# Kernel tuning notes

Hardware: AMD Instinct MI355X
Metric: run time of the kernel (lower is better)

## Reference

```python
import jax, jax.numpy as jnp
import numpy as np

K = 512
D = 256


def setup_inputs() -> dict:
    key = jax.random.key(0)
    k1, k2 = jax.random.split(key)
    x = jax.random.normal(k1, (64, D, 32, 32), dtype=jnp.float32)
    # nn.Embedding(K, D) init: uniform(-1/K, 1/K)
    emb = jax.random.uniform(k2, (K, D), dtype=jnp.float32, minval=-1.0 / K, maxval=1.0 / K)
    return {"x": x, "emb": emb}


def reference(x, emb):
    # encoder is identity: z_e_x = x, shape [B, D, H, W]
    B, Dd, H, W = x.shape
    z_e = jnp.transpose(x, (0, 2, 3, 1))           # [B, H, W, D]
    z_flat = z_e.reshape(-1, Dd)                    # [N, D]
    # squared euclidean distances to codebook: ||z||^2 + ||e||^2 - 2 z.e
    dist = (jnp.sum(z_flat * z_flat, axis=1, keepdims=True)
            + jnp.sum(emb * emb, axis=1)[None, :]
            - 2.0 * z_flat @ emb.T)                 # [N, K]
    idx = jnp.argmin(dist, axis=1)                  # [N]
    codes = emb[idx]                                # [N, D] gather
    codes = codes.reshape(B, H, W, Dd)
    # straight-through quantized output (value == codes)
    z_q_st = z_e + jax.lax.stop_gradient(codes - z_e)
    z_q_st = jnp.transpose(z_q_st, (0, 3, 1, 2))    # [B, D, H, W]
    # z_q_x_bar: gathered from live codebook (grads flow to emb)
    z_q_bar = jnp.transpose(codes, (0, 3, 1, 2))    # [B, D, H, W]
    # decoder is identity: x_tilde = z_q_st
    return (z_q_st, x, z_q_bar)
```

## Files before the change

kernel.cpp:

```cpp
#include <hip/hip_runtime.h>


#define B_  64
#define D_  256
#define HW_ 1024
#define K_  512

typedef __attribute__((ext_vector_type(8))) short short8;
typedef __attribute__((ext_vector_type(4))) float f32x4;

__device__ unsigned short g_ebf[K_ * D_];
__device__ float g_e2[K_];
__device__ float g_embT[D_ * K_];
__device__ int   g_idx[B_ * HW_];

__device__ __forceinline__ unsigned short f2bf(float f) {
    unsigned u = __float_as_uint(f);
    u += 0x7fffu + ((u >> 16) & 1u);
    return (unsigned short)(u >> 16);
}

__global__ void prep(const float* __restrict__ emb) {
    const int t   = threadIdx.x;
    const int row = blockIdx.x * 8 + (t >> 5);
    const int c0  = (t & 31) * 8;
    const float* rp = emb + row * D_ + c0;
    float4 a = *(const float4*)rp;
    float4 b = *(const float4*)(rp + 4);
    short8 v;
    v[0] = (short)f2bf(a.x); v[1] = (short)f2bf(a.y);
    v[2] = (short)f2bf(a.z); v[3] = (short)f2bf(a.w);
    v[4] = (short)f2bf(b.x); v[5] = (short)f2bf(b.y);
    v[6] = (short)f2bf(b.z); v[7] = (short)f2bf(b.w);
    *(short8*)(g_ebf + row * D_ + c0) = v;
    g_embT[(c0 + 0) * K_ + row] = a.x;
    g_embT[(c0 + 1) * K_ + row] = a.y;
    g_embT[(c0 + 2) * K_ + row] = a.z;
    g_embT[(c0 + 3) * K_ + row] = a.w;
    g_embT[(c0 + 4) * K_ + row] = b.x;
    g_embT[(c0 + 5) * K_ + row] = b.y;
    g_embT[(c0 + 6) * K_ + row] = b.z;
    g_embT[(c0 + 7) * K_ + row] = b.w;
    float ps = a.x*a.x + a.y*a.y + a.z*a.z + a.w*a.w
             + b.x*b.x + b.y*b.y + b.z*b.z + b.w*b.w;
    ps += __shfl_xor(ps, 1);  ps += __shfl_xor(ps, 2);
    ps += __shfl_xor(ps, 4);  ps += __shfl_xor(ps, 8);
    ps += __shfl_xor(ps, 16);
    if ((t & 31) == 0) g_e2[row] = ps;
}

__global__ __launch_bounds__(128, 4)
void vq_argmin(const float* __restrict__ x) {
    __shared__ float zc[4][32][32];
    __shared__ float mval[2][32];
    __shared__ int   midx[2][32];

    const int t   = threadIdx.x;
    const int w   = t >> 6;
    const int l   = t & 63;
    const int blk = blockIdx.x;
    const int b   = blk >> 5;
    const int hw0 = (blk & 31) << 5;
    const float* xb = x + ((size_t)b * D_) * HW_ + hw0;

    short8 zb[2][8];
    for (int r = 0; r < 2; ++r) {
#pragma unroll
        for (int gg = 0; gg < 2; ++gg) {
            const int g = 4 * r + 2 * w + gg;
#pragma unroll
            for (int it = 0; it < 4; ++it) {
                const float* gp = xb + (size_t)(32 * g + 8 * it + (l >> 3)) * HW_ + (l & 7) * 4;
                float* lp = &zc[g & 3][8 * it][0];
                __builtin_amdgcn_global_load_lds(
                    (const __attribute__((address_space(1))) unsigned int*)gp,
                    (__attribute__((address_space(3))) unsigned int*)lp,
                    16, 0, 0);
            }
        }
        __syncthreads();
#pragma unroll
        for (int g4 = 0; g4 < 4; ++g4) {
            const int g = 4 * r + g4;
#pragma unroll
            for (int t2 = 0; t2 < 2; ++t2) {
                const int p = 16 * t2 + (l & 15);
                short8 f;
#pragma unroll
                for (int j = 0; j < 8; ++j)
                    f[j] = (short)f2bf(zc[g4][(l >> 4) * 8 + j][p]);
                zb[t2][g] = f;
            }
        }
        __syncthreads();
    }

    float minv0 = 3.0e38f, minv1 = 3.0e38f;
    int   mini0 = 0,       mini1 = 0;
    short8 ea[8], eb[8];
    f32x4  e2a, e2b;
    const int ctbase = w * 16;

#define LOADE(buf, e2r, ct) do {                                              \
        const unsigned short* _p = g_ebf + ((ct) * 16 + (l & 15)) * D_        \
                                   + (l >> 4) * 8;                            \
        _Pragma("unroll")                                                     \
        for (int s = 0; s < 8; ++s) buf[s] = *(const short8*)(_p + s * 32);   \
        e2r = *(const f32x4*)(g_e2 + (ct) * 16 + (l >> 4) * 4);               \
    } while (0)

#define PROC(buf, e2v, ct) do {                                               \
        f32x4 a0 = {0.f, 0.f, 0.f, 0.f}, a1 = {0.f, 0.f, 0.f, 0.f};          \
        _Pragma("unroll")                                                     \
        for (int s = 0; s < 8; ++s) {                                         \
            a0 = __builtin_amdgcn_mfma_f32_16x16x32_bf16(buf[s], zb[0][s], a0, 0, 0, 0); \
            a1 = __builtin_amdgcn_mfma_f32_16x16x32_bf16(buf[s], zb[1][s], a1, 0, 0, 0); \
        }                                                                     \
        _Pragma("unroll")                                                     \
        for (int r = 0; r < 4; ++r) {                                         \
            const int code = (ct) * 16 + (l >> 4) * 4 + r;                    \
            const float s0 = e2v[r] - 2.0f * a0[r];                           \
            const float s1 = e2v[r] - 2.0f * a1[r];                           \
            if (s0 < minv0) { minv0 = s0; mini0 = code; }                     \
            if (s1 < minv1) { minv1 = s1; mini1 = code; }                     \
        }                                                                     \
    } while (0)

    LOADE(ea, e2a, ctbase);
    for (int c = 0; c < 16; c += 2) {
        LOADE(eb, e2b, ctbase + c + 1);
        PROC(ea, e2a, ctbase + c);
        const int cn = (c + 2 < 16) ? (ctbase + c + 2) : ctbase;
        LOADE(ea, e2a, cn);
        PROC(eb, e2b, ctbase + c + 1);
    }

    {
        float ov; int oi;
        ov = __shfl_xor(minv0, 16); oi = __shfl_xor(mini0, 16);
        if (ov < minv0 || (ov == minv0 && oi < mini0)) { minv0 = ov; mini0 = oi; }
        ov = __shfl_xor(minv0, 32); oi = __shfl_xor(mini0, 32);
        if (ov < minv0 || (ov == minv0 && oi < mini0)) { minv0 = ov; mini0 = oi; }
        ov = __shfl_xor(minv1, 16); oi = __shfl_xor(mini1, 16);
        if (ov < minv1 || (ov == minv1 && oi < mini1)) { minv1 = ov; mini1 = oi; }
        ov = __shfl_xor(minv1, 32); oi = __shfl_xor(mini1, 32);
        if (ov < minv1 || (ov == minv1 && oi < mini1)) { minv1 = ov; mini1 = oi; }
    }
    if ((l >> 4) == 0) {
        mval[w][l & 15]        = minv0; midx[w][l & 15]        = mini0;
        mval[w][16 + (l & 15)] = minv1; midx[w][16 + (l & 15)] = mini1;
    }
    __syncthreads();
    if (t < 32) {
        const float v0 = mval[0][t], v1 = mval[1][t];
        g_idx[b * HW_ + hw0 + t] = (v1 < v0) ? midx[1][t] : midx[0][t];
    }
}

__global__ __launch_bounds__(256)
void vq_scatter(const float* __restrict__ x, float* __restrict__ out0,
                float* __restrict__ out1, float* __restrict__ out2) {
    const int t   = threadIdx.x;
    const int blk = blockIdx.x;
    const int b   = blk >> 4;
    const int d0  = (blk & 15) << 4;
    const int4 mi = *(const int4*)(g_idx + b * HW_ + 4 * t);
    const size_t base = ((size_t)b * D_ + d0) * HW_ + 4 * t;
    const float* xp = x + base;
    float* p0 = out0 + base;
    float* p1 = out1 + base;
    float* p2 = out2 + base;
#pragma unroll 4
    for (int r = 0; r < 16; ++r) {
        const float* et = g_embT + (size_t)(d0 + r) * K_;
        const size_t off = (size_t)r * HW_;
        f32x4 xv = *(const f32x4*)(xp + off);
        f32x4 cv;
        cv[0] = et[mi.x]; cv[1] = et[mi.y];
        cv[2] = et[mi.z]; cv[3] = et[mi.w];
        __builtin_nontemporal_store(xv, (f32x4*)(p1 + off));
        __builtin_nontemporal_store(cv, (f32x4*)(p0 + off));
        __builtin_nontemporal_store(cv, (f32x4*)(p2 + off));
    }
}

extern "C" void kernel_launch(void* const* d_in, const int* in_sizes, int n_in,
                              void* d_out, int out_size, void* d_ws, size_t ws_size,
                              hipStream_t stream) {
    const float* x   = (const float*)d_in[0];
    const float* emb = (const float*)d_in[1];
    float* out0 = (float*)d_out;
    float* out1 = out0 + (size_t)16777216;
    float* out2 = out0 + (size_t)33554432;

    prep<<<64, 256, 0, stream>>>(emb);
    vq_argmin<<<2048, 128, 0, stream>>>(x);
    vq_scatter<<<1024, 256, 0, stream>>>(x, out0, out1, out2);
}
```

Before: 319.1 us.

## Stage codebook in swizzled LDS with double buffering; cache embT rows in scatter

The argmin kernel now uses 256-thread blocks covering 64 positions. Each wave owns 16 positions, and all four waves share a double-buffered, XOR-swizzled LDS copy of each 32-code bf16 codebook chunk, which is loaded asynchronously into LDS. Previously each wave fetched half the codebook straight from global memory into registers, and the result needed a cross-wave reduction through shared memory. The scatter kernel now copies an 8-row slice of the transposed codebook into LDS so its random gathers hit LDS instead of global memory, with twice as many blocks. The trade-offs are a block barrier per chunk and a higher LDS footprint per block.

```diff
diff --git a/kernel.cpp b/kernel.cpp
--- a/kernel.cpp
+++ b/kernel.cpp
@@ -49,135 +49,127 @@
     if ((t & 31) == 0) g_e2[row] = ps;
 }
 
-__global__ __launch_bounds__(128, 4)
+__global__ __launch_bounds__(256, 4)
 void vq_argmin(const float* __restrict__ x) {
-    __shared__ float zc[4][32][32];
-    __shared__ float mval[2][32];
-    __shared__ int   midx[2][32];
+    __shared__ unsigned short cb[2][32 * 256];
 
     const int t   = threadIdx.x;
     const int w   = t >> 6;
     const int l   = t & 63;
     const int blk = blockIdx.x;
-    const int b   = blk >> 5;
-    const int hw0 = (blk & 31) << 5;
+    const int b   = blk >> 4;
+    const int hw0 = (blk & 15) << 6;
     const float* xb = x + ((size_t)b * D_) * HW_ + hw0;
 
-    short8 zb[2][8];
-    for (int r = 0; r < 2; ++r) {
+    short8 zb[8];
+    float* xt = (float*)&cb[0][0];
+    for (int R = 0; R < 4; ++R) {
 #pragma unroll
-        for (int gg = 0; gg < 2; ++gg) {
-            const int g = 4 * r + 2 * w + gg;
-#pragma unroll
-            for (int it = 0; it < 4; ++it) {
-                const float* gp = xb + (size_t)(32 * g + 8 * it + (l >> 3)) * HW_ + (l & 7) * 4;
-                float* lp = &zc[g & 3][8 * it][0];
-                __builtin_amdgcn_global_load_lds(
-                    (const __attribute__((address_space(1))) unsigned int*)gp,
-                    (__attribute__((address_space(3))) unsigned int*)lp,
-                    16, 0, 0);
-            }
+        for (int k2 = 0; k2 < 4; ++k2) {
+            const int k  = 4 * w + k2;
+            const int dr = 4 * k + (l >> 4);
+            const float* gp = xb + (size_t)(64 * R + dr) * HW_ + (l & 15) * 4;
+            float* lp = xt + 256 * k;
+            __builtin_amdgcn_global_load_lds(
+                (const __attribute__((address_space(1))) unsigned int*)gp,
+                (__attribute__((address_space(3))) unsigned int*)lp, 16, 0, 0);
         }
         __syncthreads();
 #pragma unroll
-        for (int g4 = 0; g4 < 4; ++g4) {
-            const int g = 4 * r + g4;
+        for (int h = 0; h < 2; ++h) {
+            short8 f;
 #pragma unroll
-            for (int t2 = 0; t2 < 2; ++t2) {
-                const int p = 16 * t2 + (l & 15);
-                short8 f;
+            for (int j = 0; j < 8; ++j) {
+                const int dl = h * 32 + (l >> 4) * 8 + j;
+                f[j] = (short)f2bf(xt[dl * 64 + 16 * w + (l & 15)]);
+            }
+            zb[2 * R + h] = f;
+        }
+        __syncthreads();
+    }
+
+#define STAGEC(cc, bb) do {                                                   \
+        _Pragma("unroll")                                                     \
+        for (int k2 = 0; k2 < 4; ++k2) {                                      \
+            const int k  = 4 * w + k2;                                        \
+            const int rl = 2 * k + (l >> 5);        \
+            const unsigned short* gp = g_ebf + ((cc) * 32 + rl) * 256         \
+                                       + (((l & 31) ^ (rl & 7)) << 3);        \
+            unsigned short* lp = &cb[bb][512 * k];                            \
+            __builtin_amdgcn_global_load_lds(                                 \
+                (const __attribute__((address_space(1))) unsigned int*)gp,    \
+                (__attribute__((address_space(3))) unsigned int*)lp, 16, 0, 0);\
+        }                                                                     \
+    } while (0)
+
+    float minv = 3.0e38f;
+    int   mini = 0;
+
+    STAGEC(0, 0);
+    __syncthreads();
+    for (int c = 0; c < 16; ++c) {
+        if (c + 1 < 16) STAGEC(c + 1, (c + 1) & 1);
+        const unsigned short* cbuf = cb[c & 1];
 #pragma unroll
-                for (int j = 0; j < 8; ++j)
-                    f[j] = (short)f2bf(zc[g4][(l >> 4) * 8 + j][p]);
-                zb[t2][g] = f;
+        for (int ct2 = 0; ct2 < 2; ++ct2) {
+            f32x4 acc = {0.f, 0.f, 0.f, 0.f};
+            const int cr = ct2 * 16 + (l & 15);
+#pragma unroll
+            for (int s = 0; s < 8; ++s) {
+                const int unit = ((l >> 4) + 4 * s) ^ (cr & 7);
+                short8 a = *(const short8*)(cbuf + cr * 256 + unit * 8);
+                acc = __builtin_amdgcn_mfma_f32_16x16x32_bf16(a, zb[s], acc, 0, 0, 0);
+            }
+            const int cbase = 32 * c + 16 * ct2 + (l >> 4) * 4;
+            f32x4 e2v = *(const f32x4*)(g_e2 + cbase);
+#pragma unroll
+            for (int r = 0; r < 4; ++r) {
+                const float sv = e2v[r] - 2.0f * acc[r];
+                if (sv < minv) { minv = sv; mini = cbase + r; }
             }
         }
         __syncthreads();
     }
 
-    float minv0 = 3.0e38f, minv1 = 3.0e38f;
-    int   mini0 = 0,       mini1 = 0;
-    short8 ea[8], eb[8];
-    f32x4  e2a, e2b;
-    const int ctbase = w * 16;
-
-#define LOADE(buf, e2r, ct) do {                                              \
-        const unsigned short* _p = g_ebf + ((ct) * 16 + (l & 15)) * D_        \
-                                   + (l >> 4) * 8;                            \
-        _Pragma("unroll")                                                     \
-        for (int s = 0; s < 8; ++s) buf[s] = *(const short8*)(_p + s * 32);   \
-        e2r = *(const f32x4*)(g_e2 + (ct) * 16 + (l >> 4) * 4);               \
-    } while (0)
-
-#define PROC(buf, e2v, ct) do {                                               \
-        f32x4 a0 = {0.f, 0.f, 0.f, 0.f}, a1 = {0.f, 0.f, 0.f, 0.f};          \
-        _Pragma("unroll")                                                     \
-        for (int s = 0; s < 8; ++s) {                                         \
-            a0 = __builtin_amdgcn_mfma_f32_16x16x32_bf16(buf[s], zb[0][s], a0, 0, 0, 0); \
-            a1 = __builtin_amdgcn_mfma_f32_16x16x32_bf16(buf[s], zb[1][s], a1, 0, 0, 0); \
-        }                                                                     \
-        _Pragma("unroll")                                                     \
-        for (int r = 0; r < 4; ++r) {                                         \
-            const int code = (ct) * 16 + (l >> 4) * 4 + r;                    \
-            const float s0 = e2v[r] - 2.0f * a0[r];                           \
-            const float s1 = e2v[r] - 2.0f * a1[r];                           \
-            if (s0 < minv0) { minv0 = s0; mini0 = code; }                     \
-            if (s1 < minv1) { minv1 = s1; mini1 = code; }                     \
-        }                                                                     \
-    } while (0)
-
-    LOADE(ea, e2a, ctbase);
-    for (int c = 0; c < 16; c += 2) {
-        LOADE(eb, e2b, ctbase + c + 1);
-        PROC(ea, e2a, ctbase + c);
-        const int cn = (c + 2 < 16) ? (ctbase + c + 2) : ctbase;
-        LOADE(ea, e2a, cn);
-        PROC(eb, e2b, ctbase + c + 1);
-    }
-
     {
         float ov; int oi;
-        ov = __shfl_xor(minv0, 16); oi = __shfl_xor(mini0, 16);
-        if (ov < minv0 || (ov == minv0 && oi < mini0)) { minv0 = ov; mini0 = oi; }
-        ov = __shfl_xor(minv0, 32); oi = __shfl_xor(mini0, 32);
-        if (ov < minv0 || (ov == minv0 && oi < mini0)) { minv0 = ov; mini0 = oi; }
-        ov = __shfl_xor(minv1, 16); oi = __shfl_xor(mini1, 16);
-        if (ov < minv1 || (ov == minv1 && oi < mini1)) { minv1 = ov; mini1 = oi; }
-        ov = __shfl_xor(minv1, 32); oi = __shfl_xor(mini1, 32);
-        if (ov < minv1 || (ov == minv1 && oi < mini1)) { minv1 = ov; mini1 = oi; }
+        ov = __shfl_xor(minv, 16); oi = __shfl_xor(mini, 16);
+        if (ov < minv || (ov == minv && oi < mini)) { minv = ov; mini = oi; }
+        ov = __shfl_xor(minv, 32); oi = __shfl_xor(mini, 32);
+        if (ov < minv || (ov == minv && oi < mini)) { minv = ov; mini = oi; }
     }
-    if ((l >> 4) == 0) {
-        mval[w][l & 15]        = minv0; midx[w][l & 15]        = mini0;
-        mval[w][16 + (l & 15)] = minv1; midx[w][16 + (l & 15)] = mini1;
-    }
-    __syncthreads();
-    if (t < 32) {
-        const float v0 = mval[0][t], v1 = mval[1][t];
-        g_idx[b * HW_ + hw0 + t] = (v1 < v0) ? midx[1][t] : midx[0][t];
-    }
+    if (l < 16) g_idx[b * HW_ + hw0 + 16 * w + l] = mini;
 }
 
 __global__ __launch_bounds__(256)
 void vq_scatter(const float* __restrict__ x, float* __restrict__ out0,
                 float* __restrict__ out1, float* __restrict__ out2) {
+    __shared__ float et[8 * 512];
     const int t   = threadIdx.x;
     const int blk = blockIdx.x;
-    const int b   = blk >> 4;
-    const int d0  = (blk & 15) << 4;
+    const int b   = blk >> 5;
+    const int d0  = (blk & 31) << 3;
+    {
+        const float4* src = (const float4*)(g_embT + (size_t)d0 * K_);
+        float4* dst = (float4*)et;
+#pragma unroll
+        for (int i = 0; i < 4; ++i) dst[t + 256 * i] = src[t + 256 * i];
+    }
     const int4 mi = *(const int4*)(g_idx + b * HW_ + 4 * t);
+    __syncthreads();
     const size_t base = ((size_t)b * D_ + d0) * HW_ + 4 * t;
     const float* xp = x + base;
     float* p0 = out0 + base;
     float* p1 = out1 + base;
     float* p2 = out2 + base;
-#pragma unroll 4
-    for (int r = 0; r < 16; ++r) {
-        const float* et = g_embT + (size_t)(d0 + r) * K_;
+#pragma unroll
+    for (int r = 0; r < 8; ++r) {
+        const float* er = et + r * 512;
         const size_t off = (size_t)r * HW_;
         f32x4 xv = *(const f32x4*)(xp + off);
         f32x4 cv;
-        cv[0] = et[mi.x]; cv[1] = et[mi.y];
-        cv[2] = et[mi.z]; cv[3] = et[mi.w];
+        cv[0] = er[mi.x]; cv[1] = er[mi.y];
+        cv[2] = er[mi.z]; cv[3] = er[mi.w];
         __builtin_nontemporal_store(xv, (f32x4*)(p1 + off));
         __builtin_nontemporal_store(cv, (f32x4*)(p0 + off));
         __builtin_nontemporal_store(cv, (f32x4*)(p2 + off));
@@ -194,6 +186,6 @@
     float* out2 = out0 + (size_t)33554432;
 
     prep<<<64, 256, 0, stream>>>(emb);
-    vq_argmin<<<2048, 128, 0, stream>>>(x);
-    vq_scatter<<<1024, 256, 0, stream>>>(x, out0, out1, out2);
+    vq_argmin<<<1024, 256, 0, stream>>>(x);
+    vq_scatter<<<2048, 256, 0, stream>>>(x, out0, out1, out2);
 }
```

Result: faster. 273.7 us (-14.2%).
